# Kernel tuning notes

Hardware: AMD Instinct MI355X
Metric: run time of the kernel (lower is better)

The kernel has to match this reference:

```python
import jax, jax.numpy as jnp
import numpy as np

N = 10000
E = 320000
F_IN = 512
NHID = 32
LATENT = 16


def setup_inputs() -> dict:
    key = jax.random.key(0)
    k1, k2, k3, k4, k5 = jax.random.split(key, 5)
    x = jax.random.normal(k1, (N, F_IN), dtype=jnp.float32)
    W1 = jax.random.normal(k2, (F_IN, NHID), dtype=jnp.float32) * (1.0 / np.sqrt(F_IN))
    W2 = jax.random.normal(k3, (NHID, LATENT), dtype=jnp.float32) * (1.0 / np.sqrt(NHID))
    edge_index = jax.random.randint(k4, (2, E), 0, N, dtype=jnp.int32)
    edge_weight = jax.random.uniform(k5, (E,), dtype=jnp.float32)
    return {"x": x, "W1": W1, "W2": W2, "edge_index": edge_index,
            "edge_weight": edge_weight}


def _spmm(edge_index, edge_weight, h):
    # out[dst] += w * h[src]  (sparse normalized-adjacency matmul)
    src, dst = edge_index[0], edge_index[1]
    msgs = edge_weight[:, None] * h[src]          # [E, D] gather + scale
    return jax.ops.segment_sum(msgs, dst, num_segments=N)  # [N, D]


def reference(x, W1, W2, edge_index, edge_weight):
    # GCNConv layer 1: adj @ (x @ W1)
    h = _spmm(edge_index, edge_weight, x @ W1)    # [N, NHID]
    # GCNConv layer 2: adj @ (h @ W2)
    z = _spmm(edge_index, edge_weight, h @ W2)    # [N, LATENT]
    # Inner-product decoder: sigmoid(z @ z^T)
    adj_recon = jax.nn.sigmoid(z @ z.T)           # [N, N]
    return adj_recon, z
```

## Files before the change

### kernel.cpp

```cpp
#include <hip/hip_runtime.h>
#include <cstdint>
#include <cstddef>

#define N_NODES 10000
#define F_IN    512
#define NHID    32
#define LATENT  16

typedef float v4f __attribute__((ext_vector_type(4)));

#define OF_H0   0
#define OF_H    320000

#define G1_TILES 313
#define ZERO_BLOCKS 64
#define G1_KC 256

__global__ __launch_bounds__(256) void stage1_kernel(const float* __restrict__ x,
                                                     const float* __restrict__ W1,
                                                     float* __restrict__ h0,
                                                     float* __restrict__ h,
                                                     float* __restrict__ z) {
    __shared__ float w1s[G1_KC * NHID];

    if (blockIdx.x >= G1_TILES) {
        const int tid = (blockIdx.x - G1_TILES) * 256 + threadIdx.x;
        const int nthr = ZERO_BLOCKS * 256;
        float4* __restrict__ h4 = (float4*)h;
        float4* __restrict__ z4 = (float4*)z;
        const v4f zero = {0.f, 0.f, 0.f, 0.f};
        for (int i = tid; i < (N_NODES * NHID) / 4; i += nthr)
            *(v4f*)&h4[i] = zero;
        for (int i = tid; i < (N_NODES * LATENT) / 4; i += nthr)
            *(v4f*)&z4[i] = zero;
        return;
    }

    const int row0 = blockIdx.x * 32;
    const int rp   = threadIdx.x >> 3;
    const int cg   = (threadIdx.x & 7) * 4;
    const int gr   = min(row0 + rp, N_NODES - 1);
    const float4* __restrict__ xrow = (const float4*)(x + (size_t)gr * F_IN);

    float4 acc = make_float4(0.f, 0.f, 0.f, 0.f);

    for (int kc = 0; kc < F_IN; kc += G1_KC) {
        {
            const float4* __restrict__ wg = (const float4*)(W1 + (size_t)kc * NHID);
            float4* __restrict__ ws4 = (float4*)w1s;
            const int b = threadIdx.x * 8;
#pragma unroll
            for (int i = 0; i < 8; ++i) ws4[b + i] = wg[b + i];
        }
        __syncthreads();

        const int k4base = kc >> 2;
#pragma unroll 4
        for (int kk4 = 0; kk4 < G1_KC / 4; ++kk4) {
            const float4 xv = xrow[k4base + kk4];
            const float4 w0 = *(const float4*)&w1s[(kk4 * 4 + 0) * NHID + cg];
            const float4 w1 = *(const float4*)&w1s[(kk4 * 4 + 1) * NHID + cg];
            const float4 w2 = *(const float4*)&w1s[(kk4 * 4 + 2) * NHID + cg];
            const float4 w3 = *(const float4*)&w1s[(kk4 * 4 + 3) * NHID + cg];
            acc.x += xv.x * w0.x + xv.y * w1.x + xv.z * w2.x + xv.w * w3.x;
            acc.y += xv.x * w0.y + xv.y * w1.y + xv.z * w2.y + xv.w * w3.y;
            acc.z += xv.x * w0.z + xv.y * w1.z + xv.z * w2.z + xv.w * w3.z;
            acc.w += xv.x * w0.w + xv.y * w1.w + xv.z * w2.w + xv.w * w3.w;
        }
        __syncthreads();
    }

    if (row0 + rp < N_NODES) {
        *(float4*)&h0[(size_t)(row0 + rp) * NHID + cg] = acc;
    }
}

__global__ __launch_bounds__(256) void spmm32_kernel(const int* __restrict__ src,
                                                     const int* __restrict__ dst,
                                                     const float* __restrict__ w,
                                                     const float* __restrict__ hin,
                                                     float* __restrict__ hout,
                                                     int E) {
    const int idx = blockIdx.x * 256 + threadIdx.x;
    const int e = idx >> 5;
    const int d = idx & 31;
    if (e < E) {
        const int s = src[e];
        const int t = dst[e];
        const float val = w[e] * hin[(size_t)s * NHID + d];
        atomicAdd(&hout[(size_t)t * NHID + d], val);
    }
}

__global__ __launch_bounds__(256) void l2_fused_kernel(const int* __restrict__ src,
                                                       const int* __restrict__ dst,
                                                       const float* __restrict__ w,
                                                       const float* __restrict__ h,
                                                       const float* __restrict__ W2,
                                                       float* __restrict__ z,
                                                       int E) {
    __shared__ float w2s[NHID * LATENT];
    for (int t = threadIdx.x; t < NHID * LATENT; t += 256) w2s[t] = W2[t];
    __syncthreads();

    const int idx = blockIdx.x * 256 + threadIdx.x;
    const int e = idx >> 4;
    const int d = idx & (LATENT - 1);
    if (e < E) {
        const int s = src[e];
        const int t = dst[e];
        const float4* __restrict__ hr = (const float4*)(h + (size_t)s * NHID);
        float acc = 0.f;
#pragma unroll
        for (int k4 = 0; k4 < NHID / 4; ++k4) {
            const float4 hv = hr[k4];
            acc += hv.x * w2s[(k4 * 4 + 0) * LATENT + d]
                 + hv.y * w2s[(k4 * 4 + 1) * LATENT + d]
                 + hv.z * w2s[(k4 * 4 + 2) * LATENT + d]
                 + hv.w * w2s[(k4 * 4 + 3) * LATENT + d];
        }
        atomicAdd(&z[(size_t)t * LATENT + d], w[e] * acc);
    }
}

#define TI 40

__device__ __forceinline__ float sigmoid_fast(float x) {
    return __builtin_amdgcn_rcpf(1.0f + __expf(-x));
}

__global__ __launch_bounds__(256) void decoder_kernel(const float* __restrict__ z,
                                                      float* __restrict__ out) {
    const int j0 = (blockIdx.x * 256 + threadIdx.x) * 4;
    const int i0 = blockIdx.y * TI;
    if (j0 >= N_NODES) return;

    float4 zj[4][4];
    {
        const float4* __restrict__ zp = (const float4*)(z + (size_t)j0 * LATENT);
#pragma unroll
        for (int c = 0; c < 4; ++c)
#pragma unroll
            for (int q = 0; q < 4; ++q) zj[c][q] = zp[c * 4 + q];
    }

#pragma unroll 2
    for (int ii = 0; ii < TI; ++ii) {
        const int i = i0 + ii;
        const float4* __restrict__ zi = (const float4*)(z + (size_t)i * LATENT);
        const float4 c0 = zi[0], c1 = zi[1], c2 = zi[2], c3 = zi[3];
        v4f r;
#pragma unroll
        for (int c = 0; c < 4; ++c) {
            const float s =
                  c0.x * zj[c][0].x + c0.y * zj[c][0].y + c0.z * zj[c][0].z + c0.w * zj[c][0].w
                + c1.x * zj[c][1].x + c1.y * zj[c][1].y + c1.z * zj[c][1].z + c1.w * zj[c][1].w
                + c2.x * zj[c][2].x + c2.y * zj[c][2].y + c2.z * zj[c][2].z + c2.w * zj[c][2].w
                + c3.x * zj[c][3].x + c3.y * zj[c][3].y + c3.z * zj[c][3].z + c3.w * zj[c][3].w;
            r[c] = sigmoid_fast(s);
        }
        __builtin_nontemporal_store(r, (v4f*)(out + (size_t)i * N_NODES + j0));
    }
}

extern "C" void kernel_launch(void* const* d_in, const int* in_sizes, int n_in,
                              void* d_out, int out_size, void* d_ws, size_t ws_size,
                              hipStream_t stream) {
    const float* x  = (const float*)d_in[0];
    const float* W1 = (const float*)d_in[1];
    const float* W2 = (const float*)d_in[2];
    const int*   ei = (const int*)d_in[3];
    const float* ew = (const float*)d_in[4];
    const int E = in_sizes[3] / 2;
    const int* src = ei;
    const int* dst = ei + E;

    float* out = (float*)d_out;
    float* z   = out + (size_t)N_NODES * N_NODES;
    float* h0  = out + OF_H0;
    float* h   = out + OF_H;

    stage1_kernel<<<G1_TILES + ZERO_BLOCKS, 256, 0, stream>>>(x, W1, h0, h, z);

    spmm32_kernel<<<(E * NHID + 255) / 256, 256, 0, stream>>>(src, dst, ew, h0, h, E);

    l2_fused_kernel<<<(E * LATENT + 255) / 256, 256, 0, stream>>>(src, dst, ew, h, W2, z, E);

    dim3 dgrid((N_NODES / 4 + 255) / 256, N_NODES / TI);
    decoder_kernel<<<dgrid, 256, 0, stream>>>(z, out);
}
```

Measured before the change: 512.0 us.

## Fuse all four stages into one cooperative persistent kernel with grid syncs

```diff
diff --git a/kernel.cpp b/kernel.cpp
--- a/kernel.cpp
+++ b/kernel.cpp
@@ -1,6 +1,9 @@
 #include <hip/hip_runtime.h>
+#include <hip/hip_cooperative_groups.h>
 #include <cstdint>
 #include <cstddef>
+
+namespace cg = cooperative_groups;
 
 #define N_NODES 10000
 #define F_IN    512
@@ -11,6 +14,141 @@
 
 #define OF_H0   0
 #define OF_H    320000
+
+__device__ __forceinline__ float sigmoid_fast(float x) {
+    return __builtin_amdgcn_rcpf(1.0f + __expf(-x));
+}
+
+#define CGRID     512
+#define CG1_TILES 313
+#define CG1_KC    128
+
+__global__ __launch_bounds__(256, 4) void gae_mega_kernel(
+    const float* __restrict__ x, const float* __restrict__ W1,
+    const float* __restrict__ W2, const int* __restrict__ src,
+    const int* __restrict__ dst, const float* __restrict__ ew,
+    float* __restrict__ out, float* __restrict__ zv,
+    float* __restrict__ h0, float* __restrict__ h, int E) {
+    cg::grid_group grid = cg::this_grid();
+    __shared__ float smem[CG1_KC * NHID];
+
+    const int b   = blockIdx.x;
+    const int tid = threadIdx.x;
+
+    if (b < CG1_TILES) {
+        const int row0 = b * 32;
+        const int rp   = tid >> 3;
+        const int cg_  = (tid & 7) * 4;
+        const int gr   = min(row0 + rp, N_NODES - 1);
+        const float4* __restrict__ xrow = (const float4*)(x + (size_t)gr * F_IN);
+
+        float4 acc = make_float4(0.f, 0.f, 0.f, 0.f);
+        for (int kc = 0; kc < F_IN; kc += CG1_KC) {
+            {
+                const float4* __restrict__ wg = (const float4*)(W1 + (size_t)kc * NHID);
+                float4* __restrict__ ws4 = (float4*)smem;
+                const int base = tid * 4;
+#pragma unroll
+                for (int i = 0; i < 4; ++i) ws4[base + i] = wg[base + i];
+            }
+            __syncthreads();
+            const int k4base = kc >> 2;
+#pragma unroll 4
+            for (int kk4 = 0; kk4 < CG1_KC / 4; ++kk4) {
+                const float4 xv = xrow[k4base + kk4];
+                const float4 w0 = *(const float4*)&smem[(kk4 * 4 + 0) * NHID + cg_];
+                const float4 w1 = *(const float4*)&smem[(kk4 * 4 + 1) * NHID + cg_];
+                const float4 w2 = *(const float4*)&smem[(kk4 * 4 + 2) * NHID + cg_];
+                const float4 w3 = *(const float4*)&smem[(kk4 * 4 + 3) * NHID + cg_];
+                acc.x += xv.x * w0.x + xv.y * w1.x + xv.z * w2.x + xv.w * w3.x;
+                acc.y += xv.x * w0.y + xv.y * w1.y + xv.z * w2.y + xv.w * w3.y;
+                acc.z += xv.x * w0.z + xv.y * w1.z + xv.z * w2.z + xv.w * w3.z;
+                acc.w += xv.x * w0.w + xv.y * w1.w + xv.z * w2.w + xv.w * w3.w;
+            }
+            __syncthreads();
+        }
+        if (row0 + rp < N_NODES)
+            *(float4*)&h0[(size_t)(row0 + rp) * NHID + cg_] = acc;
+    } else {
+        const int t    = (b - CG1_TILES) * 256 + tid;
+        const int nthr = (CGRID - CG1_TILES) * 256;
+        const v4f zero = {0.f, 0.f, 0.f, 0.f};
+        for (int i = t; i < (N_NODES * NHID) / 4; i += nthr)
+            *(v4f*)&((float4*)h)[i] = zero;
+        for (int i = t; i < (N_NODES * LATENT) / 4; i += nthr)
+            *(v4f*)&((float4*)zv)[i] = zero;
+    }
+    grid.sync();
+
+    {
+        const int total  = E * NHID;
+        const int stride = CGRID * 256;
+        for (int idx = b * 256 + tid; idx < total; idx += stride) {
+            const int e = idx >> 5;
+            const int d = idx & 31;
+            const float val = ew[e] * h0[(size_t)src[e] * NHID + d];
+            atomicAdd(&h[(size_t)dst[e] * NHID + d], val);
+        }
+    }
+    grid.sync();
+
+    {
+        for (int t = tid; t < NHID * LATENT; t += 256) smem[t] = W2[t];
+        __syncthreads();
+        const int total  = E * LATENT;
+        const int stride = CGRID * 256;
+        for (int idx = b * 256 + tid; idx < total; idx += stride) {
+            const int e = idx >> 4;
+            const int d = idx & (LATENT - 1);
+            const float4* __restrict__ hr = (const float4*)(h + (size_t)src[e] * NHID);
+            float acc = 0.f;
+#pragma unroll
+            for (int k4 = 0; k4 < NHID / 4; ++k4) {
+                const float4 hv = hr[k4];
+                acc += hv.x * smem[(k4 * 4 + 0) * LATENT + d]
+                     + hv.y * smem[(k4 * 4 + 1) * LATENT + d]
+                     + hv.z * smem[(k4 * 4 + 2) * LATENT + d]
+                     + hv.w * smem[(k4 * 4 + 3) * LATENT + d];
+            }
+            atomicAdd(&zv[(size_t)dst[e] * LATENT + d], ew[e] * acc);
+        }
+    }
+    grid.sync();
+
+    if (b < 500) {
+        const int tx = b / 50;
+        const int i0 = (b % 50) * 200;
+        const int j0 = tx * 1024 + tid * 4;
+        if (j0 < N_NODES) {
+            float4 zj[4][4];
+            const float4* __restrict__ zp = (const float4*)(zv + (size_t)j0 * LATENT);
+#pragma unroll
+            for (int c = 0; c < 4; ++c)
+#pragma unroll
+                for (int q = 0; q < 4; ++q) zj[c][q] = zp[c * 4 + q];
+
+            float* orow = out + (size_t)i0 * N_NODES + j0;
+            const float* zrow = zv + (size_t)i0 * LATENT;
+#pragma unroll 2
+            for (int ii = 0; ii < 200; ++ii) {
+                const float4* __restrict__ zi = (const float4*)(zrow + ii * LATENT);
+                const float4 c0 = zi[0], c1 = zi[1], c2 = zi[2], c3 = zi[3];
+                v4f r;
+#pragma unroll
+                for (int c = 0; c < 4; ++c) {
+                    const float s =
+                          c0.x * zj[c][0].x + c0.y * zj[c][0].y + c0.z * zj[c][0].z + c0.w * zj[c][0].w
+                        + c1.x * zj[c][1].x + c1.y * zj[c][1].y + c1.z * zj[c][1].z + c1.w * zj[c][1].w
+                        + c2.x * zj[c][2].x + c2.y * zj[c][2].y + c2.z * zj[c][2].z + c2.w * zj[c][2].w
+                        + c3.x * zj[c][3].x + c3.y * zj[c][3].y + c3.z * zj[c][3].z + c3.w * zj[c][3].w;
+                    r[c] = sigmoid_fast(s);
+                }
+                __builtin_nontemporal_store(r, (v4f*)orow);
+                orow += N_NODES;
+            }
+        }
+    }
+}
 
 #define G1_TILES 313
 #define ZERO_BLOCKS 64
@@ -26,24 +164,21 @@
     if (blockIdx.x >= G1_TILES) {
         const int tid = (blockIdx.x - G1_TILES) * 256 + threadIdx.x;
         const int nthr = ZERO_BLOCKS * 256;
-        float4* __restrict__ h4 = (float4*)h;
-        float4* __restrict__ z4 = (float4*)z;
         const v4f zero = {0.f, 0.f, 0.f, 0.f};
         for (int i = tid; i < (N_NODES * NHID) / 4; i += nthr)
-            *(v4f*)&h4[i] = zero;
+            *(v4f*)&((float4*)h)[i] = zero;
         for (int i = tid; i < (N_NODES * LATENT) / 4; i += nthr)
-            *(v4f*)&z4[i] = zero;
+            *(v4f*)&((float4*)z)[i] = zero;
         return;
     }
 
     const int row0 = blockIdx.x * 32;
     const int rp   = threadIdx.x >> 3;
-    const int cg   = (threadIdx.x & 7) * 4;
+    const int cg_  = (threadIdx.x & 7) * 4;
     const int gr   = min(row0 + rp, N_NODES - 1);
     const float4* __restrict__ xrow = (const float4*)(x + (size_t)gr * F_IN);
 
     float4 acc = make_float4(0.f, 0.f, 0.f, 0.f);
-
     for (int kc = 0; kc < F_IN; kc += G1_KC) {
         {
             const float4* __restrict__ wg = (const float4*)(W1 + (size_t)kc * NHID);
@@ -53,15 +188,14 @@
             for (int i = 0; i < 8; ++i) ws4[b + i] = wg[b + i];
         }
         __syncthreads();
-
         const int k4base = kc >> 2;
 #pragma unroll 4
         for (int kk4 = 0; kk4 < G1_KC / 4; ++kk4) {
             const float4 xv = xrow[k4base + kk4];
-            const float4 w0 = *(const float4*)&w1s[(kk4 * 4 + 0) * NHID + cg];
-            const float4 w1 = *(const float4*)&w1s[(kk4 * 4 + 1) * NHID + cg];
-            const float4 w2 = *(const float4*)&w1s[(kk4 * 4 + 2) * NHID + cg];
-            const float4 w3 = *(const float4*)&w1s[(kk4 * 4 + 3) * NHID + cg];
+            const float4 w0 = *(const float4*)&w1s[(kk4 * 4 + 0) * NHID + cg_];
+            const float4 w1 = *(const float4*)&w1s[(kk4 * 4 + 1) * NHID + cg_];
+            const float4 w2 = *(const float4*)&w1s[(kk4 * 4 + 2) * NHID + cg_];
+            const float4 w3 = *(const float4*)&w1s[(kk4 * 4 + 3) * NHID + cg_];
             acc.x += xv.x * w0.x + xv.y * w1.x + xv.z * w2.x + xv.w * w3.x;
             acc.y += xv.x * w0.y + xv.y * w1.y + xv.z * w2.y + xv.w * w3.y;
             acc.z += xv.x * w0.z + xv.y * w1.z + xv.z * w2.z + xv.w * w3.z;
@@ -69,10 +203,8 @@
         }
         __syncthreads();
     }
-
-    if (row0 + rp < N_NODES) {
-        *(float4*)&h0[(size_t)(row0 + rp) * NHID + cg] = acc;
-    }
+    if (row0 + rp < N_NODES)
+        *(float4*)&h0[(size_t)(row0 + rp) * NHID + cg_] = acc;
 }
 
 __global__ __launch_bounds__(256) void spmm32_kernel(const int* __restrict__ src,
@@ -85,10 +217,8 @@
     const int e = idx >> 5;
     const int d = idx & 31;
     if (e < E) {
-        const int s = src[e];
-        const int t = dst[e];
-        const float val = w[e] * hin[(size_t)s * NHID + d];
-        atomicAdd(&hout[(size_t)t * NHID + d], val);
+        const float val = w[e] * hin[(size_t)src[e] * NHID + d];
+        atomicAdd(&hout[(size_t)dst[e] * NHID + d], val);
     }
 }
 
@@ -107,9 +237,7 @@
     const int e = idx >> 4;
     const int d = idx & (LATENT - 1);
     if (e < E) {
-        const int s = src[e];
-        const int t = dst[e];
-        const float4* __restrict__ hr = (const float4*)(h + (size_t)s * NHID);
+        const float4* __restrict__ hr = (const float4*)(h + (size_t)src[e] * NHID);
         float acc = 0.f;
 #pragma unroll
         for (int k4 = 0; k4 < NHID / 4; ++k4) {
@@ -119,16 +247,11 @@
                  + hv.z * w2s[(k4 * 4 + 2) * LATENT + d]
                  + hv.w * w2s[(k4 * 4 + 3) * LATENT + d];
         }
-        atomicAdd(&z[(size_t)t * LATENT + d], w[e] * acc);
+        atomicAdd(&z[(size_t)dst[e] * LATENT + d], w[e] * acc);
     }
 }
 
 #define TI 40
-
-__device__ __forceinline__ float sigmoid_fast(float x) {
-    return __builtin_amdgcn_rcpf(1.0f + __expf(-x));
-}
-
 __global__ __launch_bounds__(256) void decoder_kernel(const float* __restrict__ z,
                                                       float* __restrict__ out) {
     const int j0 = (blockIdx.x * 256 + threadIdx.x) * 4;
@@ -143,7 +266,6 @@
 #pragma unroll
             for (int q = 0; q < 4; ++q) zj[c][q] = zp[c * 4 + q];
     }
-
 #pragma unroll 2
     for (int ii = 0; ii < TI; ++ii) {
         const int i = i0 + ii;
@@ -171,21 +293,27 @@
     const float* W2 = (const float*)d_in[2];
     const int*   ei = (const int*)d_in[3];
     const float* ew = (const float*)d_in[4];
-    const int E = in_sizes[3] / 2;
+    int E = in_sizes[3] / 2;
     const int* src = ei;
     const int* dst = ei + E;
 
     float* out = (float*)d_out;
-    float* z   = out + (size_t)N_NODES * N_NODES;
+    float* zv  = out + (size_t)N_NODES * N_NODES;
     float* h0  = out + OF_H0;
     float* h   = out + OF_H;
 
-    stage1_kernel<<<G1_TILES + ZERO_BLOCKS, 256, 0, stream>>>(x, W1, h0, h, z);
-
-    spmm32_kernel<<<(E * NHID + 255) / 256, 256, 0, stream>>>(src, dst, ew, h0, h, E);
-
-    l2_fused_kernel<<<(E * LATENT + 255) / 256, 256, 0, stream>>>(src, dst, ew, h, W2, z, E);
-
-    dim3 dgrid((N_NODES / 4 + 255) / 256, N_NODES / TI);
-    decoder_kernel<<<dgrid, 256, 0, stream>>>(z, out);
-}
+    void* args[] = {(void*)&x, (void*)&W1, (void*)&W2, (void*)&src, (void*)&dst,
+                    (void*)&ew, (void*)&out, (void*)&zv, (void*)&h0, (void*)&h,
+                    (void*)&E};
+    hipError_t err = hipLaunchCooperativeKernel((const void*)gae_mega_kernel,
+                                                dim3(CGRID), dim3(256), args, 0,
+                                                stream);
+    if (err != hipSuccess) {
+        (void)hipGetLastError();
+        stage1_kernel<<<G1_TILES + ZERO_BLOCKS, 256, 0, stream>>>(x, W1, h0, h, zv);
+        spmm32_kernel<<<(E * NHID + 255) / 256, 256, 0, stream>>>(src, dst, ew, h0, h, E);
+        l2_fused_kernel<<<(E * LATENT + 255) / 256, 256, 0, stream>>>(src, dst, ew, h, W2, zv, E);
+        dim3 dgrid((N_NODES / 4 + 255) / 256, N_NODES / TI);
+        decoder_kernel<<<dgrid, 256, 0, stream>>>(zv, out);
+    }
+}
```

After: 730.4 us. 1.43x slower.
